# Kernel tuning notes

Measured on AMD Instinct MI355X. Metric: run time of the kernel, lower is better.

The kernel has to match this reference:

```python
import jax, jax.numpy as jnp
import numpy as np

B, S, D, H, L = 64, 512, 1024, 1024, 2


def setup_inputs() -> dict:
    key = jax.random.key(0)
    ks = jax.random.split(key, 12)
    x = jax.random.normal(ks[0], (B, S, D), dtype=jnp.float32)
    lengths = jax.random.randint(ks[1], (B,), 1, S + 1)
    lengths = lengths.at[0].set(S)  # ensure max len == S (matches torch trim)
    x_mask = (jnp.arange(S)[None, :] < lengths[:, None]).astype(jnp.float32)
    h0 = jax.random.normal(ks[2], (L, B, H), dtype=jnp.float32)
    sc = 1.0 / np.sqrt(H)
    p = {}
    p['Wih0'] = jax.random.uniform(ks[3], (3 * H, D), jnp.float32, -sc, sc)
    p['Whh0'] = jax.random.uniform(ks[4], (3 * H, H), jnp.float32, -sc, sc)
    p['bih0'] = jax.random.uniform(ks[5], (3 * H,), jnp.float32, -sc, sc)
    p['bhh0'] = jax.random.uniform(ks[6], (3 * H,), jnp.float32, -sc, sc)
    p['Wih1'] = jax.random.uniform(ks[7], (3 * H, H), jnp.float32, -sc, sc)
    p['Whh1'] = jax.random.uniform(ks[8], (3 * H, H), jnp.float32, -sc, sc)
    p['bih1'] = jax.random.uniform(ks[9], (3 * H,), jnp.float32, -sc, sc)
    p['bhh1'] = jax.random.uniform(ks[10], (3 * H,), jnp.float32, -sc, sc)
    return dict(x=x, x_mask=x_mask, h0=h0, **p)


def _gru_cell(xt, h, Wih, Whh, bih, bhh):
    # PyTorch gate order: r, z, n
    gi = xt @ Wih.T + bih          # [B, 3H]
    gh = h @ Whh.T + bhh           # [B, 3H]
    ir, iz, inn = jnp.split(gi, 3, axis=-1)
    hr, hz, hn = jnp.split(gh, 3, axis=-1)
    r = jax.nn.sigmoid(ir + hr)
    z = jax.nn.sigmoid(iz + hz)
    n = jnp.tanh(inn + r * hn)
    return (1.0 - z) * n + z * h


def reference(x, x_mask, h0, Wih0, Whh0, bih0, bhh0, Wih1, Whh1, bih1, bhh1):
    params = [(Wih0, Whh0, bih0, bhh0), (Wih1, Whh1, bih1, bhh1)]
    xs = jnp.swapaxes(x, 0, 1)        # [S, B, D]
    ms = x_mask.T                     # [S, B]

    def step(h, inp):
        xt, mt = inp                  # [B, D], [B]
        gate = (mt > 0.5)[:, None]    # packed seq: skip padded steps
        layer_in = xt
        new_hs = []
        for l, (Wih, Whh, bih, bhh) in enumerate(params):
            hl = h[l]
            hl_new = jnp.where(gate, _gru_cell(layer_in, hl, Wih, Whh, bih, bhh), hl)
            new_hs.append(hl_new)
            layer_in = hl_new
        h_new = jnp.stack(new_hs)
        return h_new, new_hs[-1] * mt[:, None]  # masked top-layer output

    h_final, outs = jax.lax.scan(step, h0, (xs, ms))
    output_pad = jnp.swapaxes(outs, 0, 1)        # [B, S, H]
    hidden = jnp.swapaxes(h_final, 0, 1)         # [B, L, H]
    return jnp.concatenate([output_pad, hidden], axis=1).mean(axis=1, keepdims=True)
```

## Files before the change

### kernel.cpp

```cpp
#include <hip/hip_runtime.h>
#include <hip/hip_fp16.h>

#define BB 64
#define SS 512
#define DD 1024
#define HH 1024
#define NBLK 128
#define HMASK 63

typedef _Float16 f16;
typedef unsigned long long u64;
typedef __attribute__((ext_vector_type(8))) _Float16 f16x8;
typedef __attribute__((ext_vector_type(4))) _Float16 f16x4;
typedef __attribute__((ext_vector_type(4))) float f32x4;

struct GruWS {
  unsigned sigT[4 * 32 * 16];
  f16 gi0[4][3 * HH][BB];
  f16 gi1[4][3 * HH][BB];
  f16 h0h[64][BB][HH];
  f16 h1h[64][BB][HH];
};

__device__ __forceinline__ f16x8 ld_dev_16B(const void* p) {
  f16x8 r;
  asm volatile("global_load_dwordx4 %0, %1, off sc0" : "=v"(r) : "v"(p) : "memory");
  return r;
}
__device__ __forceinline__ void st_sys_16B(void* p, f16x8 v) {
  asm volatile("global_store_dwordx4 %0, %1, off sc0 sc1" :: "v"(p), "v"(v) : "memory");
}
__device__ __forceinline__ void st_mall_16B(void* p, f16x8 v) {
  union { f16x8 v; u64 q[2]; } u; u.v = v;
  asm volatile("global_atomic_swap_x2 %0, %1, off sc1" :: "v"((u64*)p), "v"(u.q[0]) : "memory");
  asm volatile("global_atomic_swap_x2 %0, %1, off sc1" :: "v"((u64*)p + 1), "v"(u.q[1]) : "memory");
}
__device__ __forceinline__ void st_mall_8B(void* p, u64 q) {
  asm volatile("global_atomic_swap_x2 %0, %1, off sc1" :: "v"((u64*)p), "v"(q) : "memory");
}
__device__ __forceinline__ void sig_swap(unsigned* p, unsigned v) {
  asm volatile("global_atomic_swap %0, %1, off sc1" :: "v"(p), "v"(v) : "memory");
}
__device__ __forceinline__ void drain_vm() {
  asm volatile("s_waitcnt vmcnt(0)" ::: "memory");
  __builtin_amdgcn_sched_barrier(0);
}
__device__ __forceinline__ f16x4 ld_sys_f16x4(const f16* p) {
  u64 q = __hip_atomic_load((const u64*)p, __ATOMIC_RELAXED, __HIP_MEMORY_SCOPE_SYSTEM);
  union { u64 q; f16x4 v; } u; u.q = q; return u.v;
}
__device__ __forceinline__ float ld_sys_f16s(const f16* p) {
  unsigned short s = __hip_atomic_load((const unsigned short*)p, __ATOMIC_RELAXED, __HIP_MEMORY_SCOPE_SYSTEM);
  union { unsigned short s; f16 h; } u; u.s = s; return (float)u.h;
}
__device__ __forceinline__ void st_sys_u16(f16* p, f16 v) {
  union { f16 h; unsigned short s; } u; u.h = v;
  __hip_atomic_store((unsigned short*)p, u.s, __ATOMIC_RELAXED, __HIP_MEMORY_SCOPE_SYSTEM);
}
__device__ __forceinline__ void nap(int it) {
  if (it < 3) __builtin_amdgcn_s_sleep(1);
  else        __builtin_amdgcn_s_sleep(16);
}

__device__ __forceinline__ void wait1(const unsigned* p, int target, int& seen) {
  if (target <= 0 || seen >= target) return;
  int it = 0;
  for (;;) {
    unsigned v;
    asm volatile("global_load_dword %0, %1, off sc0 sc1" : "=v"(v) : "v"(p));
    asm volatile("s_waitcnt vmcnt(0)" ::: "memory");
    if ((int)v >= target) { seen = (int)v; break; }
    nap(++it);
  }
  asm volatile("" ::: "memory");
}

__device__ __forceinline__ void wait32(const unsigned* rowbase, int target, int lane, int& seen) {
  if (target <= 0 || seen >= target) return;
  const unsigned* p = rowbase + (lane & 31) * 16;
  int it = 0;
  unsigned v;
  for (;;) {
    asm volatile("global_load_dword %0, %1, off sc0 sc1" : "=v"(v) : "v"(p));
    asm volatile("s_waitcnt vmcnt(0)" ::: "memory");
    if (__all((int)v >= target)) break;
    nap(++it);
  }
  int m = (int)v;
#pragma unroll
  for (int off = 1; off < 32; off <<= 1) {
    int o = __shfl_xor(m, off);
    m = (o < m) ? o : m;
  }
  seen = m;
  asm volatile("" ::: "memory");
}

__device__ __forceinline__ void wait_hot8(const unsigned* sig, int hbase, int wv,
                                          int htgt, int giline, int gitgt,
                                          int lane, int& seenh, int& seengi) {
  const bool needh = (htgt > 0) && (seenh < htgt);
  const bool needg = (giline >= 0) && (seengi < gitgt);
  if (!needh && !needg) return;
  const bool isgi = (lane == 8) && (giline >= 0);
  const unsigned* p = sig + ((isgi ? giline : (hbase + wv * 8 + (lane & 7))) << 4);
  const int tgt = isgi ? gitgt : htgt;
  int it = 0;
  unsigned v;
  for (;;) {
    asm volatile("global_load_dword %0, %1, off sc0 sc1" : "=v"(v) : "v"(p));
    asm volatile("s_waitcnt vmcnt(0)" ::: "memory");
    if (__all((int)v >= tgt)) break;
    nap(++it);
  }
  int m = (int)v;
#pragma unroll
  for (int off = 1; off < 8; off <<= 1) {
    int o = __shfl_xor(m, off);
    m = (o < m) ? o : m;
  }
  int hmin = __shfl(m, 0);
  int gv = __shfl((int)v, 8);
  if (htgt > 0) seenh = hmin;
  if (giline >= 0) seengi = gv;
  asm volatile("" ::: "memory");
}

__global__ void gru_init(const float* __restrict__ h0, GruWS* __restrict__ ws) {
  int i = blockIdx.x * 256 + threadIdx.x;
  int j = i * 4;
  if (j < 2 * BB * HH) {
    union { f16 h[4]; u64 q; } u;
#pragma unroll
    for (int k = 0; k < 4; ++k) u.h[k] = (f16)h0[j + k];
    if (j < BB * HH) st_mall_8B(&ws->h0h[HMASK][0][j], u.q);
    else             st_mall_8B(&ws->h1h[HMASK][0][j - BB * HH], u.q);
  }
  if (i < 4 * 32)
    __hip_atomic_store(&ws->sigT[i * 16], 0u, __ATOMIC_RELAXED, __HIP_MEMORY_SCOPE_SYSTEM);
}

__device__ __forceinline__ void mma_pass(const f16x8 areg[8][4], const f16x8* bnt,
                                         float* red, int lane, int wave, f32x4 acc[3]) {
  f32x4 pacc[4][3];
#pragma unroll
  for (int m = 0; m < 4; ++m)
#pragma unroll
    for (int g = 0; g < 3; ++g) pacc[m][g] = (f32x4){0.f, 0.f, 0.f, 0.f};
#pragma unroll
  for (int kk = 0; kk < 8; ++kk)
#pragma unroll
    for (int m = 0; m < 4; ++m)
#pragma unroll
      for (int g = 0; g < 3; ++g)
        pacc[m][g] = __builtin_amdgcn_mfma_f32_16x16x32_f16(areg[kk][m], bnt[g * 8 + kk], pacc[m][g], 0, 0, 0);
#pragma unroll
  for (int m = 0; m < 4; ++m)
    if (m != wave)
#pragma unroll
      for (int g = 0; g < 3; ++g)
#pragma unroll
        for (int r = 0; r < 4; ++r)
          red[(((wave * 4 + m) * 3 + g) * 4 + r) * 64 + lane] = pacc[m][g][r];
  __syncthreads();
#pragma unroll
  for (int g = 0; g < 3; ++g) {
    f32x4 a = pacc[wave][g];
#pragma unroll
    for (int sw = 0; sw < 4; ++sw)
      if (sw != wave)
#pragma unroll
        for (int r = 0; r < 4; ++r)
          a[r] += red[(((sw * 4 + wave) * 3 + g) * 4 + r) * 64 + lane];
    acc[g] = a;
  }
}

__global__ __launch_bounds__(256, 1) void gru_main(
    const float* __restrict__ x, const float* __restrict__ xmask,
    const float* __restrict__ h0in,
    const float* __restrict__ Wih0, const float* __restrict__ Whh0,
    const float* __restrict__ bih0, const float* __restrict__ bhh0,
    const float* __restrict__ Wih1, const float* __restrict__ Whh1,
    const float* __restrict__ bih1, const float* __restrict__ bhh1,
    float* __restrict__ out, GruWS* __restrict__ ws) {
  __shared__ __align__(16) char ldsbuf[49152];
  float* red = (float*)ldsbuf;

  const int bid = blockIdx.x;
  const int grp = bid >> 5;
  const int gidx = bid & 31;
  const int base = gidx * 32;
  const int tid = threadIdx.x;
  const int lane = tid & 63;
  const int wave = tid >> 6;
  const int l15 = lane & 15;
  const int kgrp = lane >> 4;
  const int b0 = wave * 16 + kgrp * 4;
  const int kbase0 = wave * 256 + kgrp * 8;
  unsigned* sig = ws->sigT;
  unsigned* mysig = &sig[(grp * 32 + gidx) * 16];

  const float* Wsrc = (grp == 0) ? Wih0 : (grp == 1) ? Whh0 : (grp == 2) ? Wih1 : Whh1;
  f16x8 breg[2][3][8];
#pragma unroll
  for (int nt = 0; nt < 2; ++nt)
#pragma unroll
    for (int g = 0; g < 3; ++g)
#pragma unroll
      for (int kk = 0; kk < 8; ++kk) {
        const float* p = Wsrc + (long)(g * HH + base + nt * 16 + l15) * DD + kbase0 + kk * 32;
        float4 v0 = *(const float4*)p;
        float4 v1 = *(const float4*)(p + 4);
        f16x8 t;
        t[0] = (f16)v0.x; t[1] = (f16)v0.y; t[2] = (f16)v0.z; t[3] = (f16)v0.w;
        t[4] = (f16)v1.x; t[5] = (f16)v1.y; t[6] = (f16)v1.z; t[7] = (f16)v1.w;
        breg[nt][g][kk] = t;
      }

  if (grp == 0 || grp == 2) {
    const int layer = (grp == 2);
    const float* bih = layer ? bih1 : bih0;
    const float* bhh = layer ? bhh1 : bhh0;
    float bias[2][3];
#pragma unroll
    for (int nt = 0; nt < 2; ++nt)
#pragma unroll
      for (int g = 0; g < 3; ++g) {
        int colg = base + nt * 16 + l15;
        bias[nt][g] = bih[g * HH + colg] + (g < 2 ? bhh[g * HH + colg] : 0.0f);
      }
    int seen_slot = 0, seen_h = 0, dum = 0;

    for (int s = 0; s < SS; ++s) {
      if (!layer) {
        wait1(&sig[(1 * 32 + gidx) * 16], s - 3, seen_slot);
      } else {
        wait1(&sig[(3 * 32 + gidx) * 16], s - 3, seen_slot);
        wait_hot8(sig, 1 * 32, wave, s + 1, -1, 0, lane, seen_h, dum);
      }
      if ((s & 31) == 0) __threadfence();
      {
        f16x8 areg[8][4];
        if (!layer) {
#pragma unroll
          for (int kk = 0; kk < 8; ++kk)
#pragma unroll
            for (int m = 0; m < 4; ++m) {
              const float* p = x + (long)(m * 16 + l15) * (SS * DD) + (long)s * DD + kbase0 + kk * 32;
              float4 v0 = *(const float4*)p;
              float4 v1 = *(const float4*)(p + 4);
              f16x8 a;
              a[0] = (f16)v0.x; a[1] = (f16)v0.y; a[2] = (f16)v0.z; a[3] = (f16)v0.w;
              a[4] = (f16)v1.x; a[5] = (f16)v1.y; a[6] = (f16)v1.z; a[7] = (f16)v1.w;
              areg[kk][m] = a;
            }
        } else {
          const f16* A = &ws->h0h[s & HMASK][0][0];
#pragma unroll
          for (int kk = 0; kk < 8; ++kk)
#pragma unroll
            for (int m = 0; m < 4; ++m)
              areg[kk][m] = ld_dev_16B(A + (long)(m * 16 + l15) * HH + kbase0 + kk * 32);
        }
        drain_vm();
        f32x4 accs[2][3];
        mma_pass(areg, &breg[0][0][0], red, lane, wave, accs[0]);
        __syncthreads();
        mma_pass(areg, &breg[1][0][0], red, lane, wave, accs[1]);
        __syncthreads();

        f16* gt = (f16*)ldsbuf;
#pragma unroll
        for (int nt = 0; nt < 2; ++nt)
#pragma unroll
          for (int g = 0; g < 3; ++g) {
            f16x4 o;
#pragma unroll
            for (int r = 0; r < 4; ++r) o[r] = (f16)(accs[nt][g][r] + bias[nt][g]);
            *(f16x4*)(gt + (g * 32 + nt * 16 + l15) * 64 + b0) = o;
          }
        __syncthreads();
        f16* gib = layer ? &ws->gi1[s & 3][0][0] : &ws->gi0[s & 3][0][0];
#pragma unroll
        for (int rnd = 0; rnd < 3; ++rnd) {
          int idx = rnd * 256 + tid;
          int row = idx >> 3, ch = idx & 7;
          int g = row >> 5, c = row & 31;
          f16x8 v = *(const f16x8*)(gt + row * 64 + ch * 8);
          st_sys_16B(gib + (long)(g * HH + base + c) * BB + ch * 8, v);
        }
      }
      asm volatile("s_waitcnt vmcnt(0)" ::: "memory");
      __syncthreads();
      if (tid == 0) sig_swap(mysig, (unsigned)(s + 1));
    }
  } else {
    const int layer = (grp == 3);
    const float* bhh = layer ? bhh1 : bhh0;
    float bhn[2], hold[2][4], osum[2][4];
#pragma unroll
    for (int nt = 0; nt < 2; ++nt) {
      bhn[nt] = bhh[2 * HH + base + nt * 16 + l15];
#pragma unroll
      for (int r = 0; r < 4; ++r) {
        hold[nt][r] = h0in[(long)layer * BB * HH + (long)(b0 + r) * HH + base + nt * 16 + l15];
        osum[nt][r] = 0.f;
      }
    }
    int seen_gi = 0, seen_peers = 0, seen_cons = 0;

    for (int s = 0; s < SS; ++s) {
      float mv[4];
#pragma unroll
      for (int r = 0; r < 4; ++r) mv[r] = xmask[(long)(b0 + r) * SS + s];
      if (!layer) {
        wait32(&sig[2 * 32 * 16], s - 60, lane, seen_cons);
        wait_hot8(sig, 1 * 32, wave, s, 0 * 32 + gidx, s + 1, lane, seen_peers, seen_gi);
      } else {
        wait_hot8(sig, 3 * 32, wave, s, 2 * 32 + gidx, s + 1, lane, seen_peers, seen_gi);
      }
      if ((s & 31) == 0) __threadfence();
      {
        const f16* hprev = layer ? &ws->h1h[(s - 1) & HMASK][0][0] : &ws->h0h[(s - 1) & HMASK][0][0];
        const f16* gib = layer ? &ws->gi1[s & 3][0][0] : &ws->gi0[s & 3][0][0];
        f16x8 areg[8][4];
#pragma unroll
        for (int kk = 0; kk < 8; ++kk)
#pragma unroll
          for (int m = 0; m < 4; ++m)
            areg[kk][m] = ld_dev_16B(hprev + (long)(m * 16 + l15) * HH + kbase0 + kk * 32);
        f16x4 gfr[2][3];
#pragma unroll
        for (int nt = 0; nt < 2; ++nt)
#pragma unroll
          for (int g = 0; g < 3; ++g)
            gfr[nt][g] = ld_sys_f16x4(gib + (long)(g * HH + base + nt * 16 + l15) * BB + b0);
        drain_vm();

        f32x4 accs[2][3];
        mma_pass(areg, &breg[0][0][0], red, lane, wave, accs[0]);
        __syncthreads();
        mma_pass(areg, &breg[1][0][0], red, lane, wave, accs[1]);
        __syncthreads();

        f16* htile = (f16*)ldsbuf;
#pragma unroll
        for (int nt = 0; nt < 2; ++nt)
#pragma unroll
          for (int r = 0; r < 4; ++r) {
            float pr = accs[nt][0][r] + (float)gfr[nt][0][r];
            float pz = accs[nt][1][r] + (float)gfr[nt][1][r];
            float ph = accs[nt][2][r] + bhn[nt];
            float rr = 1.0f / (1.0f + __expf(-pr));
            float zz = 1.0f / (1.0f + __expf(-pz));
            float nn = tanhf((float)gfr[nt][2][r] + rr * ph);
            float upd = hold[nt][r] + (1.0f - zz) * (nn - hold[nt][r]);
            if (mv[r] > 0.5f) {
              hold[nt][r] = upd;
              if (layer) osum[nt][r] += upd;
            }
            htile[(b0 + r) * 32 + nt * 16 + l15] = (f16)hold[nt][r];
          }
        __syncthreads();
        f16* hout = layer ? &ws->h1h[s & HMASK][0][0] : &ws->h0h[s & HMASK][0][0];
        {
          int b = tid >> 2, ch = tid & 3;
          f16x8 v = *(const f16x8*)(htile + b * 32 + ch * 8);
          st_mall_16B(hout + (long)b * HH + base + ch * 8, v);
        }
        if (s == SS - 1 && layer) {
#pragma unroll
          for (int nt = 0; nt < 2; ++nt)
#pragma unroll
            for (int r = 0; r < 4; ++r) {
              int colg = base + nt * 16 + l15;
              float h0f = ld_sys_f16s(&ws->h0h[HMASK][b0 + r][colg]);
              out[(long)(b0 + r) * HH + colg] =
                  (osum[nt][r] + hold[nt][r] + h0f) * (1.0f / 514.0f);
            }
        }
      }
      asm volatile("s_waitcnt vmcnt(0)" ::: "memory");
      __syncthreads();
      if (tid == 0) sig_swap(mysig, (unsigned)(s + 1));
    }
  }
}

extern "C" void kernel_launch(void* const* d_in, const int* in_sizes, int n_in,
                              void* d_out, int out_size, void* d_ws, size_t ws_size,
                              hipStream_t stream) {
  const float* x = (const float*)d_in[0];
  const float* xmask = (const float*)d_in[1];
  const float* h0 = (const float*)d_in[2];
  const float* Wih0 = (const float*)d_in[3];
  const float* Whh0 = (const float*)d_in[4];
  const float* bih0 = (const float*)d_in[5];
  const float* bhh0 = (const float*)d_in[6];
  const float* Wih1 = (const float*)d_in[7];
  const float* Whh1 = (const float*)d_in[8];
  const float* bih1 = (const float*)d_in[9];
  const float* bhh1 = (const float*)d_in[10];
  float* out = (float*)d_out;
  GruWS* ws = (GruWS*)d_ws;

  hipLaunchKernelGGL(gru_init, dim3(128), dim3(256), 0, stream, h0, ws);
  hipLaunchKernelGGL(gru_main, dim3(NBLK), dim3(256), 0, stream,
                     x, xmask, h0, Wih0, Whh0, bih0, bhh0,
                     Wih1, Whh1, bih1, bhh1, out, ws);
}
```

Measured before the change: 9.311 ms.

## Place GRU recurrence blocks on one XCD and use local-scope signalling

Launches 256 blocks and keeps only those with bid&7 < 4. Under round-robin block placement across XCDs this should put each group's recurrent blocks on the same XCDs, so hidden-state exchange between peers can use device-local stores and atomics (h0loc/h1loc, sigL) instead of system-scope MALL traffic. If the local signal is not seen after many polls, it falls back to the global signal. The input-gate ring buffer grows from 4 to 8 slots for more producer slack, and the initial h0 is read directly from fp32 input instead of being staged by the init kernel. The placement assumption is not guaranteed, and the fallback path adds complexity and a risk to correctness.

```diff
diff --git a/kernel.cpp b/kernel.cpp
--- a/kernel.cpp
+++ b/kernel.cpp
@@ -5,8 +5,10 @@
 #define SS 512
 #define DD 1024
 #define HH 1024
-#define NBLK 128
+#define NBLK 256
 #define HMASK 63
+#define LMASK 3
+#define GMASK 7
 
 typedef _Float16 f16;
 typedef unsigned long long u64;
@@ -16,10 +18,12 @@
 
 struct GruWS {
   unsigned sigT[4 * 32 * 16];
-  f16 gi0[4][3 * HH][BB];
-  f16 gi1[4][3 * HH][BB];
-  f16 h0h[64][BB][HH];
-  f16 h1h[64][BB][HH];
+  unsigned sigL[2 * 32 * 16];
+  f16 gi0[8][3 * HH][BB];
+  f16 gi1[8][3 * HH][BB];
+  f16 h0t[64][BB][HH];
+  f16 h0loc[4][BB][HH];
+  f16 h1loc[4][BB][HH];
 };
 
 __device__ __forceinline__ f16x8 ld_dev_16B(const void* p) {
@@ -27,6 +31,9 @@
   asm volatile("global_load_dwordx4 %0, %1, off sc0" : "=v"(r) : "v"(p) : "memory");
   return r;
 }
+__device__ __forceinline__ void st_loc_16B(void* p, f16x8 v) {
+  asm volatile("global_store_dwordx4 %0, %1, off sc0" :: "v"(p), "v"(v) : "memory");
+}
 __device__ __forceinline__ void st_sys_16B(void* p, f16x8 v) {
   asm volatile("global_store_dwordx4 %0, %1, off sc0 sc1" :: "v"(p), "v"(v) : "memory");
 }
@@ -35,11 +42,11 @@
   asm volatile("global_atomic_swap_x2 %0, %1, off sc1" :: "v"((u64*)p), "v"(u.q[0]) : "memory");
   asm volatile("global_atomic_swap_x2 %0, %1, off sc1" :: "v"((u64*)p + 1), "v"(u.q[1]) : "memory");
 }
-__device__ __forceinline__ void st_mall_8B(void* p, u64 q) {
-  asm volatile("global_atomic_swap_x2 %0, %1, off sc1" :: "v"((u64*)p), "v"(q) : "memory");
-}
 __device__ __forceinline__ void sig_swap(unsigned* p, unsigned v) {
   asm volatile("global_atomic_swap %0, %1, off sc1" :: "v"(p), "v"(v) : "memory");
+}
+__device__ __forceinline__ void sigl_swap(unsigned* p, unsigned v) {
+  asm volatile("global_atomic_swap %0, %1, off" :: "v"(p), "v"(v) : "memory");
 }
 __device__ __forceinline__ void drain_vm() {
   asm volatile("s_waitcnt vmcnt(0)" ::: "memory");
@@ -52,10 +59,6 @@
 __device__ __forceinline__ float ld_sys_f16s(const f16* p) {
   unsigned short s = __hip_atomic_load((const unsigned short*)p, __ATOMIC_RELAXED, __HIP_MEMORY_SCOPE_SYSTEM);
   union { unsigned short s; f16 h; } u; u.s = s; return (float)u.h;
-}
-__device__ __forceinline__ void st_sys_u16(f16* p, f16 v) {
-  union { f16 h; unsigned short s; } u; u.h = v;
-  __hip_atomic_store((unsigned short*)p, u.s, __ATOMIC_RELAXED, __HIP_MEMORY_SCOPE_SYSTEM);
 }
 __device__ __forceinline__ void nap(int it) {
   if (it < 3) __builtin_amdgcn_s_sleep(1);
@@ -74,7 +77,6 @@
   }
   asm volatile("" ::: "memory");
 }
-
 __device__ __forceinline__ void wait32(const unsigned* rowbase, int target, int lane, int& seen) {
   if (target <= 0 || seen >= target) return;
   const unsigned* p = rowbase + (lane & 31) * 16;
@@ -95,49 +97,55 @@
   seen = m;
   asm volatile("" ::: "memory");
 }
-
 __device__ __forceinline__ void wait_hot8(const unsigned* sig, int hbase, int wv,
-                                          int htgt, int giline, int gitgt,
-                                          int lane, int& seenh, int& seengi) {
-  const bool needh = (htgt > 0) && (seenh < htgt);
-  const bool needg = (giline >= 0) && (seengi < gitgt);
-  if (!needh && !needg) return;
-  const bool isgi = (lane == 8) && (giline >= 0);
-  const unsigned* p = sig + ((isgi ? giline : (hbase + wv * 8 + (lane & 7))) << 4);
-  const int tgt = isgi ? gitgt : htgt;
+                                          int htgt, int lane, int& seenh) {
+  if (htgt <= 0 || seenh >= htgt) return;
+  const unsigned* p = sig + ((hbase + wv * 8 + (lane & 7)) << 4);
   int it = 0;
   unsigned v;
   for (;;) {
     asm volatile("global_load_dword %0, %1, off sc0 sc1" : "=v"(v) : "v"(p));
     asm volatile("s_waitcnt vmcnt(0)" ::: "memory");
-    if (__all((int)v >= tgt)) break;
+    if (__all((int)v >= htgt)) break;
     nap(++it);
   }
   int m = (int)v;
 #pragma unroll
-  for (int off = 1; off < 8; off <<= 1) {
-    int o = __shfl_xor(m, off);
-    m = (o < m) ? o : m;
-  }
-  int hmin = __shfl(m, 0);
-  int gv = __shfl((int)v, 8);
-  if (htgt > 0) seenh = hmin;
-  if (giline >= 0) seengi = gv;
+  for (int off = 1; off < 8; off <<= 1) { int o = __shfl_xor(m, off); m = (o < m) ? o : m; }
+  seenh = __shfl(m, 0);
   asm volatile("" ::: "memory");
 }
-
-__global__ void gru_init(const float* __restrict__ h0, GruWS* __restrict__ ws) {
-  int i = blockIdx.x * 256 + threadIdx.x;
-  int j = i * 4;
-  if (j < 2 * BB * HH) {
-    union { f16 h[4]; u64 q; } u;
-#pragma unroll
-    for (int k = 0; k < 4; ++k) u.h[k] = (f16)h0[j + k];
-    if (j < BB * HH) st_mall_8B(&ws->h0h[HMASK][0][j], u.q);
-    else             st_mall_8B(&ws->h1h[HMASK][0][j - BB * HH], u.q);
-  }
-  if (i < 4 * 32)
-    __hip_atomic_store(&ws->sigT[i * 16], 0u, __ATOMIC_RELAXED, __HIP_MEMORY_SCOPE_SYSTEM);
+__device__ __forceinline__ void wait8L(const unsigned* sigL, const unsigned* sigTrow,
+                                       int r13, int wv, int target, int lane, int& seen) {
+  if (target <= 0 || seen >= target) return;
+  const unsigned* p = sigL + ((r13 * 32 + wv * 8 + (lane & 7)) << 4);
+  int it = 0;
+  unsigned v;
+  for (;;) {
+    asm volatile("global_load_dword %0, %1, off sc0" : "=v"(v) : "v"(p));
+    asm volatile("s_waitcnt vmcnt(0)" ::: "memory");
+    if (__all((int)v >= target)) break;
+    if (++it > 64) {
+      int d = seen;
+      wait32(sigTrow, target, lane, d);
+      seen = d;
+      return;
+    }
+    nap(it);
+  }
+  int m = (int)v;
+#pragma unroll
+  for (int off = 1; off < 8; off <<= 1) { int o = __shfl_xor(m, off); m = (o < m) ? o : m; }
+  seen = __shfl(m, 0);
+  asm volatile("" ::: "memory");
+}
+
+__global__ void gru_fence() { __threadfence(); }
+
+__global__ void gru_init(GruWS* __restrict__ ws) {
+  int i = threadIdx.x;
+  if (i < 128) __hip_atomic_store(&ws->sigT[i * 16], 0u, __ATOMIC_RELAXED, __HIP_MEMORY_SCOPE_SYSTEM);
+  if (i < 64)  __hip_atomic_store(&ws->sigL[i * 16], 0u, __ATOMIC_RELAXED, __HIP_MEMORY_SCOPE_SYSTEM);
 }
 
 __device__ __forceinline__ void mma_pass(const f16x8 areg[8][4], const f16x8* bnt,
@@ -184,12 +192,13 @@
     const float* __restrict__ Wih1, const float* __restrict__ Whh1,
     const float* __restrict__ bih1, const float* __restrict__ bhh1,
     float* __restrict__ out, GruWS* __restrict__ ws) {
+  const int bid = blockIdx.x;
+  const int grp = bid & 7;
+  if (grp >= 4) return;
   __shared__ __align__(16) char ldsbuf[49152];
   float* red = (float*)ldsbuf;
 
-  const int bid = blockIdx.x;
-  const int grp = bid >> 5;
-  const int gidx = bid & 31;
+  const int gidx = bid >> 3;
   const int base = gidx * 32;
   const int tid = threadIdx.x;
   const int lane = tid & 63;
@@ -230,16 +239,16 @@
         int colg = base + nt * 16 + l15;
         bias[nt][g] = bih[g * HH + colg] + (g < 2 ? bhh[g * HH + colg] : 0.0f);
       }
-    int seen_slot = 0, seen_h = 0, dum = 0;
+    int seen_slot = 0, seen_h = 0;
 
     for (int s = 0; s < SS; ++s) {
       if (!layer) {
-        wait1(&sig[(1 * 32 + gidx) * 16], s - 3, seen_slot);
+        wait1(&sig[(1 * 32 + gidx) * 16], s - (GMASK - 1), seen_slot);
       } else {
-        wait1(&sig[(3 * 32 + gidx) * 16], s - 3, seen_slot);
-        wait_hot8(sig, 1 * 32, wave, s + 1, -1, 0, lane, seen_h, dum);
-      }
-      if ((s & 31) == 0) __threadfence();
+        wait1(&sig[(3 * 32 + gidx) * 16], s - (GMASK - 1), seen_slot);
+        wait_hot8(sig, 1 * 32, wave, s + 1, lane, seen_h);
+        if ((s & 31) == 0) __threadfence();
+      }
       {
         f16x8 areg[8][4];
         if (!layer) {
@@ -256,7 +265,7 @@
               areg[kk][m] = a;
             }
         } else {
-          const f16* A = &ws->h0h[s & HMASK][0][0];
+          const f16* A = &ws->h0t[s & HMASK][0][0];
 #pragma unroll
           for (int kk = 0; kk < 8; ++kk)
 #pragma unroll
@@ -281,7 +290,7 @@
             *(f16x4*)(gt + (g * 32 + nt * 16 + l15) * 64 + b0) = o;
           }
         __syncthreads();
-        f16* gib = layer ? &ws->gi1[s & 3][0][0] : &ws->gi0[s & 3][0][0];
+        f16* gib = layer ? &ws->gi1[s & GMASK][0][0] : &ws->gi0[s & GMASK][0][0];
 #pragma unroll
         for (int rnd = 0; rnd < 3; ++rnd) {
           int idx = rnd * 256 + tid;
@@ -297,7 +306,11 @@
     }
   } else {
     const int layer = (grp == 3);
+    const int r13 = layer ? 1 : 0;
     const float* bhh = layer ? bhh1 : bhh0;
+    unsigned* sigL = ws->sigL;
+    unsigned* mysigL = &sigL[(r13 * 32 + gidx) * 16];
+    const unsigned* peersT = &sig[(layer ? 3 : 1) * 32 * 16];
     float bhn[2], hold[2][4], osum[2][4];
 #pragma unroll
     for (int nt = 0; nt < 2; ++nt) {
@@ -314,72 +327,89 @@
       float mv[4];
 #pragma unroll
       for (int r = 0; r < 4; ++r) mv[r] = xmask[(long)(b0 + r) * SS + s];
+      wait1(&sig[((layer ? 2 : 0) * 32 + gidx) * 16], s + 1, seen_gi);
+      const f16* gib = layer ? &ws->gi1[s & GMASK][0][0] : &ws->gi0[s & GMASK][0][0];
+      f16x4 gfr[2][3];
+#pragma unroll
+      for (int nt = 0; nt < 2; ++nt)
+#pragma unroll
+        for (int g = 0; g < 3; ++g)
+          gfr[nt][g] = ld_sys_f16x4(gib + (long)(g * HH + base + nt * 16 + l15) * BB + b0);
+      if (!layer && wave == 0)
+        wait32(&sig[2 * 32 * 16], s - 60, lane, seen_cons);
+      wait8L(sigL, peersT, r13, wave, s, lane, seen_peers);
+
+      f16x8 areg[8][4];
+      if (s == 0) {
+        const float* A0 = h0in + (long)layer * BB * HH;
+#pragma unroll
+        for (int kk = 0; kk < 8; ++kk)
+#pragma unroll
+          for (int m = 0; m < 4; ++m) {
+            const float* p = A0 + (long)(m * 16 + l15) * HH + kbase0 + kk * 32;
+            float4 v0 = *(const float4*)p;
+            float4 v1 = *(const float4*)(p + 4);
+            f16x8 a;
+            a[0] = (f16)v0.x; a[1] = (f16)v0.y; a[2] = (f16)v0.z; a[3] = (f16)v0.w;
+            a[4] = (f16)v1.x; a[5] = (f16)v1.y; a[6] = (f16)v1.z; a[7] = (f16)v1.w;
+            areg[kk][m] = a;
+          }
+      } else {
+        const f16* A = layer ? &ws->h1loc[(s - 1) & LMASK][0][0] : &ws->h0loc[(s - 1) & LMASK][0][0];
+#pragma unroll
+        for (int kk = 0; kk < 8; ++kk)
+#pragma unroll
+          for (int m = 0; m < 4; ++m)
+            areg[kk][m] = ld_dev_16B(A + (long)(m * 16 + l15) * HH + kbase0 + kk * 32);
+      }
+      drain_vm();
+
+      f32x4 accs[2][3];
+      mma_pass(areg, &breg[0][0][0], red, lane, wave, accs[0]);
+      __syncthreads();
+      mma_pass(areg, &breg[1][0][0], red, lane, wave, accs[1]);
+      __syncthreads();
+
+      f16* htile = (f16*)ldsbuf;
+#pragma unroll
+      for (int nt = 0; nt < 2; ++nt)
+#pragma unroll
+        for (int r = 0; r < 4; ++r) {
+          float pr = accs[nt][0][r] + (float)gfr[nt][0][r];
+          float pz = accs[nt][1][r] + (float)gfr[nt][1][r];
+          float ph = accs[nt][2][r] + bhn[nt];
+          float rr = 1.0f / (1.0f + __expf(-pr));
+          float zz = 1.0f / (1.0f + __expf(-pz));
+          float nn = tanhf((float)gfr[nt][2][r] + rr * ph);
+          float upd = hold[nt][r] + (1.0f - zz) * (nn - hold[nt][r]);
+          if (mv[r] > 0.5f) {
+            hold[nt][r] = upd;
+            if (layer) osum[nt][r] += upd;
+          }
+          htile[(b0 + r) * 32 + nt * 16 + l15] = (f16)hold[nt][r];
+        }
+      __syncthreads();
+
+      const int b = tid >> 2, ch = tid & 3;
+      f16x8 hv = *(const f16x8*)(htile + b * 32 + ch * 8);
+      f16* hloc = layer ? &ws->h1loc[s & LMASK][0][0] : &ws->h0loc[s & LMASK][0][0];
+      st_loc_16B(hloc + (long)b * HH + base + ch * 8, hv);
+      asm volatile("s_waitcnt vmcnt(0)" ::: "memory");
+      __syncthreads();
+      if (tid == 0) sigl_swap(mysigL, (unsigned)(s + 1));
       if (!layer) {
-        wait32(&sig[2 * 32 * 16], s - 60, lane, seen_cons);
-        wait_hot8(sig, 1 * 32, wave, s, 0 * 32 + gidx, s + 1, lane, seen_peers, seen_gi);
-      } else {
-        wait_hot8(sig, 3 * 32, wave, s, 2 * 32 + gidx, s + 1, lane, seen_peers, seen_gi);
-      }
-      if ((s & 31) == 0) __threadfence();
-      {
-        const f16* hprev = layer ? &ws->h1h[(s - 1) & HMASK][0][0] : &ws->h0h[(s - 1) & HMASK][0][0];
-        const f16* gib = layer ? &ws->gi1[s & 3][0][0] : &ws->gi0[s & 3][0][0];
-        f16x8 areg[8][4];
-#pragma unroll
-        for (int kk = 0; kk < 8; ++kk)
-#pragma unroll
-          for (int m = 0; m < 4; ++m)
-            areg[kk][m] = ld_dev_16B(hprev + (long)(m * 16 + l15) * HH + kbase0 + kk * 32);
-        f16x4 gfr[2][3];
+        st_mall_16B(&ws->h0t[s & HMASK][0][0] + (long)b * HH + base + ch * 8, hv);
+      }
+      if (s == SS - 1 && layer) {
 #pragma unroll
         for (int nt = 0; nt < 2; ++nt)
 #pragma unroll
-          for (int g = 0; g < 3; ++g)
-            gfr[nt][g] = ld_sys_f16x4(gib + (long)(g * HH + base + nt * 16 + l15) * BB + b0);
-        drain_vm();
-
-        f32x4 accs[2][3];
-        mma_pass(areg, &breg[0][0][0], red, lane, wave, accs[0]);
-        __syncthreads();
-        mma_pass(areg, &breg[1][0][0], red, lane, wave, accs[1]);
-        __syncthreads();
-
-        f16* htile = (f16*)ldsbuf;
-#pragma unroll
-        for (int nt = 0; nt < 2; ++nt)
-#pragma unroll
           for (int r = 0; r < 4; ++r) {
-            float pr = accs[nt][0][r] + (float)gfr[nt][0][r];
-            float pz = accs[nt][1][r] + (float)gfr[nt][1][r];
-            float ph = accs[nt][2][r] + bhn[nt];
-            float rr = 1.0f / (1.0f + __expf(-pr));
-            float zz = 1.0f / (1.0f + __expf(-pz));
-            float nn = tanhf((float)gfr[nt][2][r] + rr * ph);
-            float upd = hold[nt][r] + (1.0f - zz) * (nn - hold[nt][r]);
-            if (mv[r] > 0.5f) {
-              hold[nt][r] = upd;
-              if (layer) osum[nt][r] += upd;
-            }
-            htile[(b0 + r) * 32 + nt * 16 + l15] = (f16)hold[nt][r];
+            int colg = base + nt * 16 + l15;
+            float h0f = ld_sys_f16s(&ws->h0t[(SS - 1) & HMASK][b0 + r][colg]);
+            out[(long)(b0 + r) * HH + colg] =
+                (osum[nt][r] + hold[nt][r] + h0f) * (1.0f / 514.0f);
           }
-        __syncthreads();
-        f16* hout = layer ? &ws->h1h[s & HMASK][0][0] : &ws->h0h[s & HMASK][0][0];
-        {
-          int b = tid >> 2, ch = tid & 3;
-          f16x8 v = *(const f16x8*)(htile + b * 32 + ch * 8);
-          st_mall_16B(hout + (long)b * HH + base + ch * 8, v);
-        }
-        if (s == SS - 1 && layer) {
-#pragma unroll
-          for (int nt = 0; nt < 2; ++nt)
-#pragma unroll
-            for (int r = 0; r < 4; ++r) {
-              int colg = base + nt * 16 + l15;
-              float h0f = ld_sys_f16s(&ws->h0h[HMASK][b0 + r][colg]);
-              out[(long)(b0 + r) * HH + colg] =
-                  (osum[nt][r] + hold[nt][r] + h0f) * (1.0f / 514.0f);
-            }
-        }
       }
       asm volatile("s_waitcnt vmcnt(0)" ::: "memory");
       __syncthreads();
@@ -405,7 +435,8 @@
   float* out = (float*)d_out;
   GruWS* ws = (GruWS*)d_ws;
 
-  hipLaunchKernelGGL(gru_init, dim3(128), dim3(256), 0, stream, h0, ws);
+  hipLaunchKernelGGL(gru_fence, dim3(64), dim3(64), 0, stream);
+  hipLaunchKernelGGL(gru_init, dim3(1), dim3(256), 0, stream, ws);
   hipLaunchKernelGGL(gru_main, dim3(NBLK), dim3(256), 0, stream,
                      x, xmask, h0, Wih0, Whh0, bih0, bhh0,
                      Wih1, Whh1, bih1, bhh1, out, ws);
```

Result: slower. 17.37 ms (+86.5%).
